# Kernel tuning notes

Hardware: AMD Instinct MI355X
Metric: run time of the kernel (lower is better)

## Reference

```python
import jax, jax.numpy as jnp
import numpy as np

B, L, E, V = 16, 2048, 1280, 32
P = V * (V - 1) // 2  # 496 upper-triangular entries
LN_EPS = 1e-12  # ESM1bLayerNorm default eps


def setup_inputs() -> dict:
    key = jax.random.key(0)
    ks = jax.random.split(key, 6)
    s = 0.02
    return {
        "hx": jax.random.normal(ks[0], (B, L, E), dtype=jnp.float32),
        "valid_token_mask": jnp.ones((V,), dtype=bool),
        # params stored (in, out) so forward is x @ W + b
        "dense_w": jax.random.normal(ks[1], (E, E), dtype=jnp.float32) * s,
        "dense_b": jnp.zeros((E,), dtype=jnp.float32),
        "ln_g": jnp.ones((E,), dtype=jnp.float32),
        "ln_b": jnp.zeros((E,), dtype=jnp.float32),
        "theta_w": jax.random.normal(ks[2], (E, V), dtype=jnp.float32) * s,
        "theta_b": jnp.zeros((V,), dtype=jnp.float32),
        "Theta_w": jax.random.normal(ks[3], (E, P), dtype=jnp.float32) * s,
        "Theta_b": jnp.zeros((P,), dtype=jnp.float32),
    }


def reference(hx, valid_token_mask, dense_w, dense_b, ln_g, ln_b,
              theta_w, theta_b, Theta_w, Theta_b):
    mask = valid_token_mask  # (V,) bool
    # dense -> gelu (exact erf, as in ESM) -> layer norm
    h = jax.nn.gelu(hx @ dense_w + dense_b, approximate=False)
    mu = h.mean(-1, keepdims=True)
    var = ((h - mu) ** 2).mean(-1, keepdims=True)
    h = (h - mu) / jnp.sqrt(var + LN_EPS) * ln_g + ln_b  # (B,L,E)

    # stationary distribution logits with invalid tokens masked to -inf
    pi_logits = h @ theta_w + theta_b  # (B,L,V)
    pi_logits = jnp.where(mask, pi_logits, -jnp.inf)
    log_pi = jax.nn.log_softmax(pi_logits, axis=-1)

    # symmetric off-diagonal rates via upper-triangular parameterization
    Theta = jax.nn.softplus(h @ Theta_w + Theta_b)  # (B,L,P)
    iu, ju = jnp.triu_indices(V, k=1)
    S = jnp.zeros((B, L, V, V), dtype=hx.dtype).at[:, :, iu, ju].set(Theta)
    S = S + S.swapaxes(-1, -2)
    mask2d = mask[:, None] & mask[None, :]
    S = S * mask2d  # zero out invalid state pairs

    # Pande transform: Q_ij = S_ij * sqrt(pi_j / pi_i) (elementwise, O(V^2))
    log_pi_safe = jnp.where(mask, log_pi, 0.0)
    pi_sqrt = jnp.exp(0.5 * log_pi_safe)  # (B,L,V)
    Q = S * (pi_sqrt[..., None, :] / pi_sqrt[..., :, None])

    # row-sum correction: Q <- Q - diag(row sums); diag of Q is zero here
    row_sum = Q.sum(-1)  # (B,L,V)
    Q = Q - jnp.eye(V, dtype=Q.dtype) * row_sum[..., :, None]

    return Q, jnp.exp(log_pi)
```

## Files before the change

### kernel.cpp

```cpp
#include <hip/hip_runtime.h>
#include <math.h>

typedef float f32x4 __attribute__((ext_vector_type(4)));
typedef short s16x8 __attribute__((ext_vector_type(8)));

static constexpr int BL = 32768;
static constexpr int E_DIM = 1280;
static constexpr int V_DIM = 32;
static constexpr int P_DIM = 496;
static constexpr int N2 = 640;

#define DEV __device__ __forceinline__

DEV unsigned short f2bf(float f) {
  unsigned u = __float_as_uint(f);
  unsigned r = (u + 0x7fffu + ((u >> 16) & 1u)) >> 16;
  return (unsigned short)r;
}
DEV float bf2f(unsigned short h) { return __uint_as_float(((unsigned)h) << 16); }

__global__ void decode_mask_kernel(const void* __restrict__ mraw, float* __restrict__ out) {
  const int t = threadIdx.x;
  const int* mi = (const int*)mraw;
  const unsigned char* mc = (const unsigned char*)mraw;
  bool ok = true;
  if (t < 8) {
    int v = mi[t];
    ok = (v == 0) || (v == 1);
  }
  unsigned long long bal = __ballot(ok);
  const bool useInt = ((bal & 0xFFull) == 0xFFull);
  if (t < 32) {
    float m;
    if (useInt) m = (mi[t] != 0) ? 1.0f : 0.0f;
    else        m = (mc[t] != 0) ? 1.0f : 0.0f;
    out[t] = m;
  }
}

__global__ __launch_bounds__(256) void build_wt1_kernel(const float* __restrict__ w,
                                                        unsigned short* __restrict__ thi,
                                                        unsigned short* __restrict__ tlo) {
  __shared__ float tile[32][33];
  const int tx = threadIdx.x & 31, ty = threadIdx.x >> 5;
  const int k0 = blockIdx.x * 32, n0 = blockIdx.y * 32;
#pragma unroll
  for (int r = ty; r < 32; r += 8) tile[r][tx] = w[(size_t)(k0 + r) * E_DIM + (n0 + tx)];
  __syncthreads();
#pragma unroll
  for (int r = ty; r < 32; r += 8) {
    float v = tile[tx][r];
    unsigned short h = f2bf(v);
    size_t o = (size_t)(n0 + r) * E_DIM + (k0 + tx);
    thi[o] = h;
    if (tlo) tlo[o] = f2bf(v - bf2f(h));
  }
}

__global__ __launch_bounds__(256) void build_wt2_kernel(const float* __restrict__ theta_w,
                                                        const float* __restrict__ Theta_w,
                                                        unsigned short* __restrict__ thi,
                                                        unsigned short* __restrict__ tlo) {
  __shared__ float tile[32][33];
  const int tx = threadIdx.x & 31, ty = threadIdx.x >> 5;
  const int k0 = blockIdx.x * 32, n0 = blockIdx.y * 32;
#pragma unroll
  for (int r = ty; r < 32; r += 8) {
    int n = n0 + tx, k = k0 + r;
    float v = 0.0f;
    if (n < V_DIM) v = theta_w[(size_t)k * V_DIM + n];
    else if (n < V_DIM + P_DIM) v = Theta_w[(size_t)k * P_DIM + (n - V_DIM)];
    tile[r][tx] = v;
  }
  __syncthreads();
#pragma unroll
  for (int r = ty; r < 32; r += 8) {
    float v = tile[tx][r];
    unsigned short h = f2bf(v);
    size_t o = (size_t)(n0 + r) * E_DIM + (k0 + tx);
    thi[o] = h;
    if (tlo) tlo[o] = f2bf(v - bf2f(h));
  }
}

__global__ void build_b2_kernel(const float* __restrict__ theta_b,
                                const float* __restrict__ Theta_b, float* __restrict__ b2) {
  int n = threadIdx.x;
  float v = 0.0f;
  if (n < V_DIM) v = theta_b[n];
  else if (n < V_DIM + P_DIM) v = Theta_b[n - V_DIM];
  b2[n] = v;
}

template <int EPI, bool LO>
__global__ __launch_bounds__(256) void gemm3_kernel(
    const float* __restrict__ Afp,
    const unsigned short* __restrict__ Ahi, const unsigned short* __restrict__ Alo,
    const unsigned short* __restrict__ Bhi, const unsigned short* __restrict__ Blo,
    const float* __restrict__ bias,
    unsigned short* __restrict__ OutHi, unsigned short* __restrict__ OutLo,
    float* __restrict__ OutF, int ldo) {
  constexpr int BM = 128, BN = 128, BK = 32, KD = 1280;
  __shared__ unsigned short Ah[BM * BK];
  __shared__ unsigned short Bh[BN * BK];
  __shared__ unsigned short Al[LO ? BM * BK : 64];
  __shared__ unsigned short Bl[LO ? BN * BK : 64];

  const int t = threadIdx.x;
  const int lane = t & 63;
  const int w = t >> 6;
  const int wm = (w >> 1) * 64;
  const int wn = (w & 1) * 64;

  unsigned flat = blockIdx.y * 256u + blockIdx.x;
  unsigned total = gridDim.x * gridDim.y;
  unsigned logical = (flat & 7u) * (total >> 3) + (flat >> 3);
  const int m0 = (int)(logical & 255u) * BM;
  const int n0 = (int)(logical >> 8) * BN;

  f32x4 acc[4][4] = {};

  const int rl = lane & 15;
  const int kb = (lane >> 4) * 8;

  for (int kt = 0; kt < KD; kt += BK) {
#pragma unroll
    for (int i = 0; i < 2; ++i) {
      int c = t + 256 * i;
      int row = c >> 2;
      int kc = (c & 3) * 8;
      size_t go = (size_t)(n0 + row) * KD + kt + kc;
      __builtin_amdgcn_global_load_lds(
          (const __attribute__((address_space(1))) unsigned int*)(Bhi + go),
          (__attribute__((address_space(3))) unsigned int*)(Bh + c * 8), 16, 0, 0);
      if constexpr (LO)
        __builtin_amdgcn_global_load_lds(
            (const __attribute__((address_space(1))) unsigned int*)(Blo + go),
            (__attribute__((address_space(3))) unsigned int*)(Bl + c * 8), 16, 0, 0);
    }
    if constexpr (EPI == 0) {
#pragma unroll
      for (int i = 0; i < 4; ++i) {
        int c = t + 256 * i;
        int row = c >> 3;
        int c4 = (c & 7) * 4;
        const float4 v = *(const float4*)(Afp + (size_t)(m0 + row) * KD + kt + c4);
        ushort4 hh;
        hh.x = f2bf(v.x); hh.y = f2bf(v.y); hh.z = f2bf(v.z); hh.w = f2bf(v.w);
        *(ushort4*)(Ah + row * BK + c4) = hh;
        if constexpr (LO) {
          ushort4 ll;
          ll.x = f2bf(v.x - bf2f(hh.x));
          ll.y = f2bf(v.y - bf2f(hh.y));
          ll.z = f2bf(v.z - bf2f(hh.z));
          ll.w = f2bf(v.w - bf2f(hh.w));
          *(ushort4*)(Al + row * BK + c4) = ll;
        }
      }
    } else {
#pragma unroll
      for (int i = 0; i < 2; ++i) {
        int c = t + 256 * i;
        int row = c >> 2;
        int kc = (c & 3) * 8;
        size_t go = (size_t)(m0 + row) * KD + kt + kc;
        __builtin_amdgcn_global_load_lds(
            (const __attribute__((address_space(1))) unsigned int*)(Ahi + go),
            (__attribute__((address_space(3))) unsigned int*)(Ah + c * 8), 16, 0, 0);
        if constexpr (LO)
          __builtin_amdgcn_global_load_lds(
              (const __attribute__((address_space(1))) unsigned int*)(Alo + go),
              (__attribute__((address_space(3))) unsigned int*)(Al + c * 8), 16, 0, 0);
      }
    }
    __syncthreads();

    s16x8 afh[4], afl[4], bfh[4], bfl[4];
#pragma unroll
    for (int mi = 0; mi < 4; ++mi) {
      int r = wm + mi * 16 + rl;
      afh[mi] = *(const s16x8*)(Ah + r * BK + kb);
      if constexpr (LO) afl[mi] = *(const s16x8*)(Al + r * BK + kb);
    }
#pragma unroll
    for (int ni = 0; ni < 4; ++ni) {
      int r = wn + ni * 16 + rl;
      bfh[ni] = *(const s16x8*)(Bh + r * BK + kb);
      if constexpr (LO) bfl[ni] = *(const s16x8*)(Bl + r * BK + kb);
    }
#pragma unroll
    for (int mi = 0; mi < 4; ++mi)
#pragma unroll
      for (int ni = 0; ni < 4; ++ni) {
        acc[mi][ni] = __builtin_amdgcn_mfma_f32_16x16x32_bf16(afh[mi], bfh[ni], acc[mi][ni], 0, 0, 0);
        if constexpr (LO) {
          acc[mi][ni] = __builtin_amdgcn_mfma_f32_16x16x32_bf16(afh[mi], bfl[ni], acc[mi][ni], 0, 0, 0);
          acc[mi][ni] = __builtin_amdgcn_mfma_f32_16x16x32_bf16(afl[mi], bfh[ni], acc[mi][ni], 0, 0, 0);
        }
      }
    __syncthreads();
  }

  const int rb = (lane >> 4) * 4;
  const int cl = lane & 15;
#pragma unroll
  for (int mi = 0; mi < 4; ++mi) {
#pragma unroll
    for (int ni = 0; ni < 4; ++ni) {
      const int gc = n0 + wn + ni * 16 + cl;
      const float bsv = bias[gc];
#pragma unroll
      for (int r = 0; r < 4; ++r) {
        const int gr = m0 + wm + mi * 16 + rb + r;
        float x = acc[mi][ni][r] + bsv;
        if constexpr (EPI == 0) {
          float g = 0.5f * x * (1.0f + erff(x * 0.7071067811865476f));
          unsigned short hh = f2bf(g);
          OutHi[(size_t)gr * ldo + gc] = hh;
          if constexpr (LO) OutLo[(size_t)gr * ldo + gc] = f2bf(g - bf2f(hh));
        } else {
          OutF[(size_t)gr * ldo + gc] = x;
        }
      }
    }
  }
}

__global__ __launch_bounds__(320) void ln_kernel(unsigned short* __restrict__ hhi,
                                                 unsigned short* __restrict__ hlo,
                                                 const float* __restrict__ gw,
                                                 const float* __restrict__ bw) {
  const size_t base = (size_t)blockIdx.x * E_DIM;
  const int t = threadIdx.x;
  const int lane = t & 63, w = t >> 6;
  const size_t off = base + (size_t)t * 4;
  const ushort4 hv = *(const ushort4*)(hhi + off);
  float v0 = bf2f(hv.x), v1 = bf2f(hv.y), v2 = bf2f(hv.z), v3 = bf2f(hv.w);
  if (hlo) {
    const ushort4 lv = *(const ushort4*)(hlo + off);
    v0 += bf2f(lv.x); v1 += bf2f(lv.y); v2 += bf2f(lv.z); v3 += bf2f(lv.w);
  }
  float s = v0 + v1 + v2 + v3;
  float sq = v0 * v0 + v1 * v1 + v2 * v2 + v3 * v3;
#pragma unroll
  for (int o = 32; o >= 1; o >>= 1) { s += __shfl_xor(s, o); sq += __shfl_xor(sq, o); }
  __shared__ float ls[5], lq[5];
  if (lane == 0) { ls[w] = s; lq[w] = sq; }
  __syncthreads();
  s = ls[0] + ls[1] + ls[2] + ls[3] + ls[4];
  sq = lq[0] + lq[1] + lq[2] + lq[3] + lq[4];
  const float mu = s * (1.0f / E_DIM);
  const float var = sq * (1.0f / E_DIM) - mu * mu;
  const float rstd = rsqrtf(var + 1e-12f);
  const float4 g4 = *(const float4*)(gw + (size_t)t * 4);
  const float4 b4 = *(const float4*)(bw + (size_t)t * 4);
  const float y0 = (v0 - mu) * rstd * g4.x + b4.x;
  const float y1 = (v1 - mu) * rstd * g4.y + b4.y;
  const float y2 = (v2 - mu) * rstd * g4.z + b4.z;
  const float y3 = (v3 - mu) * rstd * g4.w + b4.w;
  ushort4 oh;
  oh.x = f2bf(y0); oh.y = f2bf(y1); oh.z = f2bf(y2); oh.w = f2bf(y3);
  *(ushort4*)(hhi + off) = oh;
  if (hlo) {
    ushort4 ol;
    ol.x = f2bf(y0 - bf2f(oh.x));
    ol.y = f2bf(y1 - bf2f(oh.y));
    ol.z = f2bf(y2 - bf2f(oh.z));
    ol.w = f2bf(y3 - bf2f(oh.w));
    *(ushort4*)(hlo + off) = ol;
  }
}

__global__ __launch_bounds__(256) void qbuild_kernel(const float* __restrict__ g2,
                                                     const float* __restrict__ maskf,
                                                     float* __restrict__ Qout,
                                                     float* __restrict__ piOut) {
  __shared__ float sS[4][P_DIM];
  __shared__ float sR[4][V_DIM];
  __shared__ float sC[4][V_DIM];
  const int t = threadIdx.x;
  const int w = t >> 6, lane = t & 63;
  const int p = blockIdx.x * 4 + w;
  const float* row = g2 + (size_t)p * N2;

  const int c = lane & 31;
  const bool mv = maskf[c] != 0.0f;
  const float xm = mv ? row[c] : -INFINITY;
  float mx = xm;
#pragma unroll
  for (int o = 16; o >= 1; o >>= 1) mx = fmaxf(mx, __shfl_xor(mx, o, 32));
  const float e = mv ? expf(xm - mx) : 0.0f;
  float se = e;
#pragma unroll
  for (int o = 16; o >= 1; o >>= 1) se += __shfl_xor(se, o, 32);
  const float lp = xm - mx - logf(se);
  const float lps = mv ? lp : 0.0f;
  if (lane < 32) {
    piOut[(size_t)p * V_DIM + lane] = mv ? expf(lp) : 0.0f;
    sR[w][lane] = mv ? expf(-0.5f * lps) : 0.0f;
    sC[w][lane] = mv ? expf(0.5f * lps) : 0.0f;
  }
  for (int idx = lane; idx < P_DIM; idx += 64) {
    float tv = row[V_DIM + idx];
    sS[w][idx] = tv > 20.0f ? tv : log1pf(expf(tv));
  }
  __syncthreads();

#pragma unroll
  for (int t16 = 0; t16 < 16; ++t16) {
    const int eidx = t16 * 64 + lane;
    const int i = eidx >> 5, j = eidx & 31;
    float v = 0.0f;
    if (i != j) {
      const int a = i < j ? i : j;
      const int b = i < j ? j : i;
      const int pq = a * 31 - (a * (a - 1)) / 2 + (b - a - 1);
      v = sS[w][pq] * sR[w][i] * sC[w][j];
    }
    float r = v;
#pragma unroll
    for (int o = 16; o >= 1; o >>= 1) r += __shfl_xor(r, o, 32);
    Qout[(size_t)p * (V_DIM * V_DIM) + eidx] = (i == j) ? -r : v;
  }
}

extern "C" void kernel_launch(void* const* d_in, const int* in_sizes, int n_in,
                              void* d_out, int out_size, void* d_ws, size_t ws_size,
                              hipStream_t stream) {
  const float* hx = (const float*)d_in[0];
  const void* mask_raw = (const void*)d_in[1];
  const float* dense_w = (const float*)d_in[2];
  const float* dense_b = (const float*)d_in[3];
  const float* ln_g = (const float*)d_in[4];
  const float* ln_b = (const float*)d_in[5];
  const float* theta_w = (const float*)d_in[6];
  const float* theta_b = (const float*)d_in[7];
  const float* Theta_w = (const float*)d_in[8];
  const float* Theta_b = (const float*)d_in[9];

  char* ws = (char*)d_ws;
  float* g2out = (float*)(ws + 0);
  unsigned short* h_hi = (unsigned short*)(ws + 83886080ULL);
  unsigned short* wt1_hi = (unsigned short*)(ws + 167772160ULL);
  unsigned short* wt2_hi = (unsigned short*)(ws + 171048960ULL);
  float* b2 = (float*)(ws + 172687360ULL);
  float* maskf = (float*)(ws + 172689920ULL);
  const size_t FULL_NEED = 261491456ULL;
  const bool full = ws_size >= FULL_NEED;
  unsigned short* h_lo = full ? (unsigned short*)(ws + 172690176ULL) : nullptr;
  unsigned short* wt1_lo = full ? (unsigned short*)(ws + 256576256ULL) : nullptr;
  unsigned short* wt2_lo = full ? (unsigned short*)(ws + 259853056ULL) : nullptr;

  float* Qout = (float*)d_out;
  float* piOut = Qout + (size_t)BL * V_DIM * V_DIM;

  decode_mask_kernel<<<1, 64, 0, stream>>>(mask_raw, maskf);
  build_wt1_kernel<<<dim3(40, 40), 256, 0, stream>>>(dense_w, wt1_hi, wt1_lo);
  build_wt2_kernel<<<dim3(40, 20), 256, 0, stream>>>(theta_w, Theta_w, wt2_hi, wt2_lo);
  build_b2_kernel<<<1, 640, 0, stream>>>(theta_b, Theta_b, b2);

  if (full) {
    gemm3_kernel<0, true><<<dim3(256, 10), 256, 0, stream>>>(
        hx, nullptr, nullptr, wt1_hi, wt1_lo, dense_b, h_hi, h_lo, nullptr, E_DIM);
    ln_kernel<<<BL, 320, 0, stream>>>(h_hi, h_lo, ln_g, ln_b);
    gemm3_kernel<1, true><<<dim3(256, 5), 256, 0, stream>>>(
        nullptr, h_hi, h_lo, wt2_hi, wt2_lo, b2, nullptr, nullptr, g2out, N2);
  } else {
    gemm3_kernel<0, false><<<dim3(256, 10), 256, 0, stream>>>(
        hx, nullptr, nullptr, wt1_hi, nullptr, dense_b, h_hi, nullptr, nullptr, E_DIM);
    ln_kernel<<<BL, 320, 0, stream>>>(h_hi, nullptr, ln_g, ln_b);
    gemm3_kernel<1, false><<<dim3(256, 5), 256, 0, stream>>>(
        nullptr, h_hi, nullptr, wt2_hi, nullptr, b2, nullptr, nullptr, g2out, N2);
  }
  qbuild_kernel<<<8192, 256, 0, stream>>>(g2out, maskf, Qout, piOut);
}
```

Before: 987.9 us.

## Drop split-bf16 hi/lo GEMMs, pre-convert input, double-buffer LDS staging

Removes the hi/lo split-bf16 emulation, so each GEMM issues one MFMA per tile step instead of three and no longer reads or writes the low-part buffers. The fp32 input is converted to bf16 in a separate pass before the first GEMM, and the GEMM now double-buffers its LDS tiles so the next K-slice is loaded while the current one is multiplied. The LDS layout is reorganised into K-chunk-major blocks and the launch bound now requests 4 blocks per CU. In exchange, accuracy falls to plain bf16 inputs with fp32 accumulation, and the extra conversion pass adds a full read and write of the activations.

```diff
diff --git a/kernel.cpp b/kernel.cpp
--- a/kernel.cpp
+++ b/kernel.cpp
@@ -38,9 +38,21 @@
   }
 }
 
+__global__ __launch_bounds__(256) void f32_to_bf16_kernel(const float* __restrict__ in,
+                                                          unsigned short* __restrict__ out,
+                                                          int n4) {
+  int idx = blockIdx.x * 256 + threadIdx.x;
+  const int stride = gridDim.x * 256;
+  for (; idx < n4; idx += stride) {
+    const float4 v = *(const float4*)(in + (size_t)idx * 4);
+    ushort4 o;
+    o.x = f2bf(v.x); o.y = f2bf(v.y); o.z = f2bf(v.z); o.w = f2bf(v.w);
+    *(ushort4*)(out + (size_t)idx * 4) = o;
+  }
+}
+
 __global__ __launch_bounds__(256) void build_wt1_kernel(const float* __restrict__ w,
-                                                        unsigned short* __restrict__ thi,
-                                                        unsigned short* __restrict__ tlo) {
+                                                        unsigned short* __restrict__ thi) {
   __shared__ float tile[32][33];
   const int tx = threadIdx.x & 31, ty = threadIdx.x >> 5;
   const int k0 = blockIdx.x * 32, n0 = blockIdx.y * 32;
@@ -48,19 +60,13 @@
   for (int r = ty; r < 32; r += 8) tile[r][tx] = w[(size_t)(k0 + r) * E_DIM + (n0 + tx)];
   __syncthreads();
 #pragma unroll
-  for (int r = ty; r < 32; r += 8) {
-    float v = tile[tx][r];
-    unsigned short h = f2bf(v);
-    size_t o = (size_t)(n0 + r) * E_DIM + (k0 + tx);
-    thi[o] = h;
-    if (tlo) tlo[o] = f2bf(v - bf2f(h));
-  }
+  for (int r = ty; r < 32; r += 8)
+    thi[(size_t)(n0 + r) * E_DIM + (k0 + tx)] = f2bf(tile[tx][r]);
 }
 
 __global__ __launch_bounds__(256) void build_wt2_kernel(const float* __restrict__ theta_w,
                                                         const float* __restrict__ Theta_w,
-                                                        unsigned short* __restrict__ thi,
-                                                        unsigned short* __restrict__ tlo) {
+                                                        unsigned short* __restrict__ thi) {
   __shared__ float tile[32][33];
   const int tx = threadIdx.x & 31, ty = threadIdx.x >> 5;
   const int k0 = blockIdx.x * 32, n0 = blockIdx.y * 32;
@@ -74,13 +80,8 @@
   }
   __syncthreads();
 #pragma unroll
-  for (int r = ty; r < 32; r += 8) {
-    float v = tile[tx][r];
-    unsigned short h = f2bf(v);
-    size_t o = (size_t)(n0 + r) * E_DIM + (k0 + tx);
-    thi[o] = h;
-    if (tlo) tlo[o] = f2bf(v - bf2f(h));
-  }
+  for (int r = ty; r < 32; r += 8)
+    thi[(size_t)(n0 + r) * E_DIM + (k0 + tx)] = f2bf(tile[tx][r]);
 }
 
 __global__ void build_b2_kernel(const float* __restrict__ theta_b,
@@ -92,114 +93,87 @@
   b2[n] = v;
 }
 
-template <int EPI, bool LO>
-__global__ __launch_bounds__(256) void gemm3_kernel(
-    const float* __restrict__ Afp,
-    const unsigned short* __restrict__ Ahi, const unsigned short* __restrict__ Alo,
-    const unsigned short* __restrict__ Bhi, const unsigned short* __restrict__ Blo,
-    const float* __restrict__ bias,
-    unsigned short* __restrict__ OutHi, unsigned short* __restrict__ OutLo,
+template <int EPI>
+__global__ __launch_bounds__(256, 4) void gemm_bf16_kernel(
+    const unsigned short* __restrict__ A, const unsigned short* __restrict__ B,
+    const float* __restrict__ bias, unsigned short* __restrict__ OutBf,
     float* __restrict__ OutF, int ldo) {
-  constexpr int BM = 128, BN = 128, BK = 32, KD = 1280;
-  __shared__ unsigned short Ah[BM * BK];
-  __shared__ unsigned short Bh[BN * BK];
-  __shared__ unsigned short Al[LO ? BM * BK : 64];
-  __shared__ unsigned short Bl[LO ? BN * BK : 64];
+  constexpr int BK = 32, KD = 1280, NKT = KD / BK;
+  __shared__ __align__(16) unsigned short As[2][128 * BK];
+  __shared__ __align__(16) unsigned short Bs[2][128 * BK];
 
   const int t = threadIdx.x;
   const int lane = t & 63;
   const int w = t >> 6;
-  const int wm = (w >> 1) * 64;
-  const int wn = (w & 1) * 64;
+  const int wm = (w >> 1) * 64, wn = (w & 1) * 64;
 
   unsigned flat = blockIdx.y * 256u + blockIdx.x;
   unsigned total = gridDim.x * gridDim.y;
   unsigned logical = (flat & 7u) * (total >> 3) + (flat >> 3);
-  const int m0 = (int)(logical & 255u) * BM;
-  const int n0 = (int)(logical >> 8) * BN;
+  const int m0 = (int)(logical & 255u) * 128;
+  const int n0 = (int)(logical >> 8) * 128;
+
+  const int q0 = t >> 7, r0 = t & 127;
+  const int c1 = t + 256;
+  const int q1 = c1 >> 7, r1 = c1 & 127;
+  const unsigned short* a0 = A + (size_t)(m0 + r0) * KD + q0 * 8;
+  const unsigned short* a1 = A + (size_t)(m0 + r1) * KD + q1 * 8;
+  const unsigned short* b0 = B + (size_t)(n0 + r0) * KD + q0 * 8;
+  const unsigned short* b1 = B + (size_t)(n0 + r1) * KD + q1 * 8;
+
+#define STAGE(buf, kt)                                                                  \
+  do {                                                                                  \
+    __builtin_amdgcn_global_load_lds(                                                   \
+        (const __attribute__((address_space(1))) unsigned int*)(a0 + (kt)),             \
+        (__attribute__((address_space(3))) unsigned int*)(&As[(buf)][t * 8]), 16, 0, 0);\
+    __builtin_amdgcn_global_load_lds(                                                   \
+        (const __attribute__((address_space(1))) unsigned int*)(a1 + (kt)),             \
+        (__attribute__((address_space(3))) unsigned int*)(&As[(buf)][c1 * 8]), 16, 0, 0);\
+    __builtin_amdgcn_global_load_lds(                                                   \
+        (const __attribute__((address_space(1))) unsigned int*)(b0 + (kt)),             \
+        (__attribute__((address_space(3))) unsigned int*)(&Bs[(buf)][t * 8]), 16, 0, 0);\
+    __builtin_amdgcn_global_load_lds(                                                   \
+        (const __attribute__((address_space(1))) unsigned int*)(b1 + (kt)),             \
+        (__attribute__((address_space(3))) unsigned int*)(&Bs[(buf)][c1 * 8]), 16, 0, 0);\
+  } while (0)
 
   f32x4 acc[4][4] = {};
-
-  const int rl = lane & 15;
-  const int kb = (lane >> 4) * 8;
-
-  for (int kt = 0; kt < KD; kt += BK) {
-#pragma unroll
-    for (int i = 0; i < 2; ++i) {
-      int c = t + 256 * i;
-      int row = c >> 2;
-      int kc = (c & 3) * 8;
-      size_t go = (size_t)(n0 + row) * KD + kt + kc;
-      __builtin_amdgcn_global_load_lds(
-          (const __attribute__((address_space(1))) unsigned int*)(Bhi + go),
-          (__attribute__((address_space(3))) unsigned int*)(Bh + c * 8), 16, 0, 0);
-      if constexpr (LO)
-        __builtin_amdgcn_global_load_lds(
-            (const __attribute__((address_space(1))) unsigned int*)(Blo + go),
-            (__attribute__((address_space(3))) unsigned int*)(Bl + c * 8), 16, 0, 0);
-    }
-    if constexpr (EPI == 0) {
-#pragma unroll
-      for (int i = 0; i < 4; ++i) {
-        int c = t + 256 * i;
-        int row = c >> 3;
-        int c4 = (c & 7) * 4;
-        const float4 v = *(const float4*)(Afp + (size_t)(m0 + row) * KD + kt + c4);
-        ushort4 hh;
-        hh.x = f2bf(v.x); hh.y = f2bf(v.y); hh.z = f2bf(v.z); hh.w = f2bf(v.w);
-        *(ushort4*)(Ah + row * BK + c4) = hh;
-        if constexpr (LO) {
-          ushort4 ll;
-          ll.x = f2bf(v.x - bf2f(hh.x));
-          ll.y = f2bf(v.y - bf2f(hh.y));
-          ll.z = f2bf(v.z - bf2f(hh.z));
-          ll.w = f2bf(v.w - bf2f(hh.w));
-          *(ushort4*)(Al + row * BK + c4) = ll;
-        }
-      }
-    } else {
-#pragma unroll
-      for (int i = 0; i < 2; ++i) {
-        int c = t + 256 * i;
-        int row = c >> 2;
-        int kc = (c & 3) * 8;
-        size_t go = (size_t)(m0 + row) * KD + kt + kc;
-        __builtin_amdgcn_global_load_lds(
-            (const __attribute__((address_space(1))) unsigned int*)(Ahi + go),
-            (__attribute__((address_space(3))) unsigned int*)(Ah + c * 8), 16, 0, 0);
-        if constexpr (LO)
-          __builtin_amdgcn_global_load_lds(
-              (const __attribute__((address_space(1))) unsigned int*)(Alo + go),
-              (__attribute__((address_space(3))) unsigned int*)(Al + c * 8), 16, 0, 0);
-      }
-    }
+  const int q = lane >> 4, r = lane & 15;
+  const int abase = q * 1024 + (wm + r) * 8;
+  const int bbase = q * 1024 + (wn + r) * 8;
+
+  STAGE(0, 0);
+  __syncthreads();
+
+  int cur = 0;
+  for (int ki = 0; ki < NKT - 1; ++ki) {
+    STAGE(cur ^ 1, (ki + 1) * BK);
+    s16x8 af[4], bf[4];
+#pragma unroll
+    for (int mi = 0; mi < 4; ++mi) af[mi] = *(const s16x8*)(&As[cur][abase + mi * 128]);
+#pragma unroll
+    for (int ni = 0; ni < 4; ++ni) bf[ni] = *(const s16x8*)(&Bs[cur][bbase + ni * 128]);
+#pragma unroll
+    for (int mi = 0; mi < 4; ++mi)
+#pragma unroll
+      for (int ni = 0; ni < 4; ++ni)
+        acc[mi][ni] = __builtin_amdgcn_mfma_f32_16x16x32_bf16(af[mi], bf[ni], acc[mi][ni], 0, 0, 0);
     __syncthreads();
-
-    s16x8 afh[4], afl[4], bfh[4], bfl[4];
-#pragma unroll
-    for (int mi = 0; mi < 4; ++mi) {
-      int r = wm + mi * 16 + rl;
-      afh[mi] = *(const s16x8*)(Ah + r * BK + kb);
-      if constexpr (LO) afl[mi] = *(const s16x8*)(Al + r * BK + kb);
-    }
-#pragma unroll
-    for (int ni = 0; ni < 4; ++ni) {
-      int r = wn + ni * 16 + rl;
-      bfh[ni] = *(const s16x8*)(Bh + r * BK + kb);
-      if constexpr (LO) bfl[ni] = *(const s16x8*)(Bl + r * BK + kb);
-    }
+    cur ^= 1;
+  }
+  {
+    s16x8 af[4], bf[4];
+#pragma unroll
+    for (int mi = 0; mi < 4; ++mi) af[mi] = *(const s16x8*)(&As[cur][abase + mi * 128]);
+#pragma unroll
+    for (int ni = 0; ni < 4; ++ni) bf[ni] = *(const s16x8*)(&Bs[cur][bbase + ni * 128]);
 #pragma unroll
     for (int mi = 0; mi < 4; ++mi)
 #pragma unroll
-      for (int ni = 0; ni < 4; ++ni) {
-        acc[mi][ni] = __builtin_amdgcn_mfma_f32_16x16x32_bf16(afh[mi], bfh[ni], acc[mi][ni], 0, 0, 0);
-        if constexpr (LO) {
-          acc[mi][ni] = __builtin_amdgcn_mfma_f32_16x16x32_bf16(afh[mi], bfl[ni], acc[mi][ni], 0, 0, 0);
-          acc[mi][ni] = __builtin_amdgcn_mfma_f32_16x16x32_bf16(afl[mi], bfh[ni], acc[mi][ni], 0, 0, 0);
-        }
-      }
-    __syncthreads();
-  }
+      for (int ni = 0; ni < 4; ++ni)
+        acc[mi][ni] = __builtin_amdgcn_mfma_f32_16x16x32_bf16(af[mi], bf[ni], acc[mi][ni], 0, 0, 0);
+  }
+#undef STAGE
 
   const int rb = (lane >> 4) * 4;
   const int cl = lane & 15;
@@ -210,14 +184,12 @@
       const int gc = n0 + wn + ni * 16 + cl;
       const float bsv = bias[gc];
 #pragma unroll
-      for (int r = 0; r < 4; ++r) {
-        const int gr = m0 + wm + mi * 16 + rb + r;
-        float x = acc[mi][ni][r] + bsv;
+      for (int rr = 0; rr < 4; ++rr) {
+        const int gr = m0 + wm + mi * 16 + rb + rr;
+        float x = acc[mi][ni][rr] + bsv;
         if constexpr (EPI == 0) {
           float g = 0.5f * x * (1.0f + erff(x * 0.7071067811865476f));
-          unsigned short hh = f2bf(g);
-          OutHi[(size_t)gr * ldo + gc] = hh;
-          if constexpr (LO) OutLo[(size_t)gr * ldo + gc] = f2bf(g - bf2f(hh));
+          OutBf[(size_t)gr * ldo + gc] = f2bf(g);
         } else {
           OutF[(size_t)gr * ldo + gc] = x;
         }
@@ -226,20 +198,15 @@
   }
 }
 
-__global__ __launch_bounds__(320) void ln_kernel(unsigned short* __restrict__ hhi,
-                                                 unsigned short* __restrict__ hlo,
+__global__ __launch_bounds__(320) void ln_kernel(unsigned short* __restrict__ h,
                                                  const float* __restrict__ gw,
                                                  const float* __restrict__ bw) {
   const size_t base = (size_t)blockIdx.x * E_DIM;
   const int t = threadIdx.x;
   const int lane = t & 63, w = t >> 6;
   const size_t off = base + (size_t)t * 4;
-  const ushort4 hv = *(const ushort4*)(hhi + off);
-  float v0 = bf2f(hv.x), v1 = bf2f(hv.y), v2 = bf2f(hv.z), v3 = bf2f(hv.w);
-  if (hlo) {
-    const ushort4 lv = *(const ushort4*)(hlo + off);
-    v0 += bf2f(lv.x); v1 += bf2f(lv.y); v2 += bf2f(lv.z); v3 += bf2f(lv.w);
-  }
+  const ushort4 hv = *(const ushort4*)(h + off);
+  const float v0 = bf2f(hv.x), v1 = bf2f(hv.y), v2 = bf2f(hv.z), v3 = bf2f(hv.w);
   float s = v0 + v1 + v2 + v3;
   float sq = v0 * v0 + v1 * v1 + v2 * v2 + v3 * v3;
 #pragma unroll
@@ -254,21 +221,12 @@
   const float rstd = rsqrtf(var + 1e-12f);
   const float4 g4 = *(const float4*)(gw + (size_t)t * 4);
   const float4 b4 = *(const float4*)(bw + (size_t)t * 4);
-  const float y0 = (v0 - mu) * rstd * g4.x + b4.x;
-  const float y1 = (v1 - mu) * rstd * g4.y + b4.y;
-  const float y2 = (v2 - mu) * rstd * g4.z + b4.z;
-  const float y3 = (v3 - mu) * rstd * g4.w + b4.w;
   ushort4 oh;
-  oh.x = f2bf(y0); oh.y = f2bf(y1); oh.z = f2bf(y2); oh.w = f2bf(y3);
-  *(ushort4*)(hhi + off) = oh;
-  if (hlo) {
-    ushort4 ol;
-    ol.x = f2bf(y0 - bf2f(oh.x));
-    ol.y = f2bf(y1 - bf2f(oh.y));
-    ol.z = f2bf(y2 - bf2f(oh.z));
-    ol.w = f2bf(y3 - bf2f(oh.w));
-    *(ushort4*)(hlo + off) = ol;
-  }
+  oh.x = f2bf((v0 - mu) * rstd * g4.x + b4.x);
+  oh.y = f2bf((v1 - mu) * rstd * g4.y + b4.y);
+  oh.z = f2bf((v2 - mu) * rstd * g4.z + b4.z);
+  oh.w = f2bf((v3 - mu) * rstd * g4.w + b4.w);
+  *(ushort4*)(h + off) = oh;
 }
 
 __global__ __launch_bounds__(256) void qbuild_kernel(const float* __restrict__ g2,
@@ -317,10 +275,10 @@
       const int pq = a * 31 - (a * (a - 1)) / 2 + (b - a - 1);
       v = sS[w][pq] * sR[w][i] * sC[w][j];
     }
-    float r = v;
-#pragma unroll
-    for (int o = 16; o >= 1; o >>= 1) r += __shfl_xor(r, o, 32);
-    Qout[(size_t)p * (V_DIM * V_DIM) + eidx] = (i == j) ? -r : v;
+    float rsum = v;
+#pragma unroll
+    for (int o = 16; o >= 1; o >>= 1) rsum += __shfl_xor(rsum, o, 32);
+    Qout[(size_t)p * (V_DIM * V_DIM) + eidx] = (i == j) ? -rsum : v;
   }
 }
 
@@ -339,38 +297,25 @@
   const float* Theta_b = (const float*)d_in[9];
 
   char* ws = (char*)d_ws;
+  unsigned short* hx_bf = (unsigned short*)(ws + 0);
   float* g2out = (float*)(ws + 0);
-  unsigned short* h_hi = (unsigned short*)(ws + 83886080ULL);
-  unsigned short* wt1_hi = (unsigned short*)(ws + 167772160ULL);
-  unsigned short* wt2_hi = (unsigned short*)(ws + 171048960ULL);
+  unsigned short* h_bf = (unsigned short*)(ws + 83886080ULL);
+  unsigned short* wt1 = (unsigned short*)(ws + 167772160ULL);
+  unsigned short* wt2 = (unsigned short*)(ws + 171048960ULL);
   float* b2 = (float*)(ws + 172687360ULL);
   float* maskf = (float*)(ws + 172689920ULL);
-  const size_t FULL_NEED = 261491456ULL;
-  const bool full = ws_size >= FULL_NEED;
-  unsigned short* h_lo = full ? (unsigned short*)(ws + 172690176ULL) : nullptr;
-  unsigned short* wt1_lo = full ? (unsigned short*)(ws + 256576256ULL) : nullptr;
-  unsigned short* wt2_lo = full ? (unsigned short*)(ws + 259853056ULL) : nullptr;
 
   float* Qout = (float*)d_out;
   float* piOut = Qout + (size_t)BL * V_DIM * V_DIM;
 
   decode_mask_kernel<<<1, 64, 0, stream>>>(mask_raw, maskf);
-  build_wt1_kernel<<<dim3(40, 40), 256, 0, stream>>>(dense_w, wt1_hi, wt1_lo);
-  build_wt2_kernel<<<dim3(40, 20), 256, 0, stream>>>(theta_w, Theta_w, wt2_hi, wt2_lo);
+  build_wt1_kernel<<<dim3(40, 40), 256, 0, stream>>>(dense_w, wt1);
+  build_wt2_kernel<<<dim3(40, 20), 256, 0, stream>>>(theta_w, Theta_w, wt2);
   build_b2_kernel<<<1, 640, 0, stream>>>(theta_b, Theta_b, b2);
-
-  if (full) {
-    gemm3_kernel<0, true><<<dim3(256, 10), 256, 0, stream>>>(
-        hx, nullptr, nullptr, wt1_hi, wt1_lo, dense_b, h_hi, h_lo, nullptr, E_DIM);
-    ln_kernel<<<BL, 320, 0, stream>>>(h_hi, h_lo, ln_g, ln_b);
-    gemm3_kernel<1, true><<<dim3(256, 5), 256, 0, stream>>>(
-        nullptr, h_hi, h_lo, wt2_hi, wt2_lo, b2, nullptr, nullptr, g2out, N2);
-  } else {
-    gemm3_kernel<0, false><<<dim3(256, 10), 256, 0, stream>>>(
-        hx, nullptr, nullptr, wt1_hi, nullptr, dense_b, h_hi, nullptr, nullptr, E_DIM);
-    ln_kernel<<<BL, 320, 0, stream>>>(h_hi, nullptr, ln_g, ln_b);
-    gemm3_kernel<1, false><<<dim3(256, 5), 256, 0, stream>>>(
-        nullptr, h_hi, nullptr, wt2_hi, nullptr, b2, nullptr, nullptr, g2out, N2);
-  }
+  f32_to_bf16_kernel<<<2048, 256, 0, stream>>>(hx, hx_bf, BL * E_DIM / 4);
+
+  gemm_bf16_kernel<0><<<dim3(256, 10), 256, 0, stream>>>(hx_bf, wt1, dense_b, h_bf, nullptr, E_DIM);
+  ln_kernel<<<BL, 320, 0, stream>>>(h_bf, ln_g, ln_b);
+  gemm_bf16_kernel<1><<<dim3(256, 5), 256, 0, stream>>>(h_bf, wt2, b2, nullptr, g2out, N2);
   qbuild_kernel<<<8192, 256, 0, stream>>>(g2out, maskf, Qout, piOut);
 }
```

Measured after the change: 908.2 us. -8.1%, faster.
